# Optimization experiments

Hardware: AMD Instinct MI355X
Metric: run time of the kernel (lower is better)

## Reference

```python
import jax, jax.numpy as jnp
import numpy as np

B, T, H, V = 256, 256, 512, 32000
L = 3  # stacked LSTM layers


def setup_inputs() -> dict:
    key = jax.random.key(0)
    ks = jax.random.split(key, 12)
    s = 0.05
    n = lambda k, shp: (jax.random.normal(k, shp, jnp.float32) * s)
    return {
        "text_1": jax.random.randint(ks[0], (B, T), 0, V, dtype=jnp.int32),
        "text_2": jax.random.randint(ks[1], (B, T), 0, V, dtype=jnp.int32),
        "text_3": jax.random.randint(ks[2], (B, T), 0, V, dtype=jnp.int32),
        "emb": n(ks[3], (V, H)),
        "Wx": n(ks[4], (L, H, 4 * H)),
        "Wh": n(ks[5], (L, H, 4 * H)),
        "b": jnp.zeros((L, 4 * H), jnp.float32),
        "g1": jnp.ones((3 * H,), jnp.float32), "beta1": jnp.zeros((3 * H,), jnp.float32),
        "W1": n(ks[6], (3 * H, 2 * H)), "bd1": jnp.zeros((2 * H,), jnp.float32),
        "g2": jnp.ones((2 * H,), jnp.float32), "beta2": jnp.zeros((2 * H,), jnp.float32),
        "W2": n(ks[7], (2 * H, H // 5)), "bd2": jnp.zeros((H // 5,), jnp.float32),
        "g3": jnp.ones((H // 5,), jnp.float32), "beta3": jnp.zeros((H // 5,), jnp.float32),
        "W3": n(ks[8], (H // 5, 4)), "bd3": jnp.zeros((4,), jnp.float32),
    }


def _lstm_stack(tokens, emb, Wx, Wh, b):
    # tokens: [B, T] int -> last hidden of top layer [B, H]
    x = emb[tokens]                      # [B, T, H]
    x = jnp.transpose(x, (1, 0, 2))      # [T, B, H] (scan over time)
    bsz, h = x.shape[1], Wh.shape[1]
    for l in range(Wx.shape[0]):
        Wx_l, Wh_l, b_l = Wx[l], Wh[l], b[l]
        def step(carry, xt):
            hprev, cprev = carry
            gates = xt @ Wx_l + hprev @ Wh_l + b_l      # [B, 4H]
            i, f, g, o = jnp.split(gates, 4, axis=-1)
            c = jax.nn.sigmoid(f) * cprev + jax.nn.sigmoid(i) * jnp.tanh(g)
            hnew = jax.nn.sigmoid(o) * jnp.tanh(c)
            return (hnew, c), hnew
        init = (jnp.zeros((bsz, h), x.dtype), jnp.zeros((bsz, h), x.dtype))
        _, x = jax.lax.scan(step, init, x)
    return x[-1]                          # rnn_output[:, -1, :]


def _bn(x, gamma, beta, eps=1e-3):
    m = jnp.mean(x, axis=0)
    v = jnp.var(x, axis=0)
    return gamma * (x - m) * jax.lax.rsqrt(v + eps) + beta


def reference(text_1, text_2, text_3, emb, Wx, Wh, b,
              g1, beta1, W1, bd1, g2, beta2, W2, bd2, g3, beta3, W3, bd3):
    r1 = _lstm_stack(text_1, emb, Wx, Wh, b)
    r2 = _lstm_stack(text_2, emb, Wx, Wh, b)
    r3 = _lstm_stack(text_3, emb, Wx, Wh, b)
    r = jnp.concatenate([r1, r2, r3], axis=1)   # [B, 3H]
    r = _bn(r, g1, beta1)
    r = jax.nn.selu(r @ W1 + bd1)
    r = _bn(r, g2, beta2)
    r = jax.nn.selu(r @ W2 + bd2)
    r = _bn(r, g3, beta3)
    return r @ W3 + bd3                          # [B, 4] logits
```

## Files before the change

### kernel.cpp

```cpp
#include <hip/hip_runtime.h>
#include <hip/hip_bf16.h>

typedef __attribute__((ext_vector_type(8))) short short8;
typedef __attribute__((ext_vector_type(4))) float floatx4;

namespace {
constexpr int kB1 = 256;
constexpr int kT  = 256;
constexpr int kH  = 512;
constexpr int kL  = 3;
constexpr int kB3 = 768;
constexpr int kK  = 1024;
constexpr int kN  = 2048;
constexpr size_t kHB = (size_t)kB3 * kH;

constexpr size_t WREP_OFF   = 0;
constexpr size_t WREP_BYTES = (size_t)kL * kK * kN * 2;
constexpr size_t BREP_OFF   = WREP_OFF + WREP_BYTES;
constexpr size_t BREP_BYTES = (size_t)kL * kN * 4;
constexpr size_t HBUF_OFF   = BREP_OFF + BREP_BYTES;
constexpr size_t HBUF_BYTES = (size_t)kL * 2 * kHB * 2;
constexpr size_t CBUF_OFF   = HBUF_OFF + HBUF_BYTES;
constexpr size_t CBUF_BYTES = (size_t)kL * kHB * 4;
constexpr size_t BNA_OFF    = CBUF_OFF + CBUF_BYTES;
constexpr size_t BNC_OFF    = BNA_OFF + 1536 * 4;
constexpr size_t Z1_OFF     = BNC_OFF + 1536 * 4;
constexpr size_t Z2_OFF     = Z1_OFF + (size_t)256 * 1024 * 4;
constexpr size_t FLAG_OFF   = Z2_OFF + (size_t)256 * 102 * 4;
}

__device__ __forceinline__ float ldf(const void* p, size_t idx, int isf32) {
  if (isf32) return ((const float*)p)[idx];
  return __bfloat162float(((const __hip_bfloat16*)p)[idx]);
}

__device__ __forceinline__ short f2bs(float x) {
  union { __hip_bfloat16 h; short s; } u;
  u.h = __float2bfloat16(x);
  return u.s;
}

__global__ void detect_kernel(const unsigned* __restrict__ g1, int* __restrict__ flag) {
  if (threadIdx.x == 0 && blockIdx.x == 0)
    *flag = (g1[0] == 0x3F800000u) ? 1 : 0;
}

__global__ __launch_bounds__(256) void repack_kernel(
    const void* __restrict__ Wx, const void* __restrict__ Wh,
    const void* __restrict__ bias, const int* __restrict__ flagp,
    __hip_bfloat16* __restrict__ Wrep, float* __restrict__ brep) {
  int isf32 = *flagp;
  int idx = blockIdx.x * 256 + threadIdx.x;
  if (idx >= kL * kK * kN) return;
  int j  = idx & 7;
  int n2 = (idx >> 3) & (kN - 1);
  int kg = (idx >> 14) & 127;
  int l  = idx >> 21;
  int k  = kg * 8 + j;
  int ntile = n2 >> 7, c = n2 & 127, g = c >> 5, ul = c & 31;
  int u = ntile * 32 + ul;
  int col = g * 512 + u;
  float v;
  if (k < kH) v = ldf(Wx, ((size_t)l * kH + k) * kN + col, isf32);
  else        v = ldf(Wh, ((size_t)l * kH + (k - kH)) * kN + col, isf32);
  Wrep[idx] = __float2bfloat16(v);
  if (kg == 0 && j == 0) brep[l * kN + n2] = ldf(bias, (size_t)l * kN + col, isf32);
}

__global__ __launch_bounds__(256) void step_kernel(
    int s,
    const __hip_bfloat16* __restrict__ Wrep, const float* __restrict__ brep,
    __hip_bfloat16* __restrict__ hbuf, float* __restrict__ cbuf,
    const void* __restrict__ emb, const int* __restrict__ flagp,
    const int* __restrict__ t1, const int* __restrict__ t2, const int* __restrict__ t3) {
  __shared__ __align__(16) char smem[34816];

  int bid = blockIdx.x;
  int l  = bid / 192;
  int rr = bid % 192;
  int nt = rr & 15;
  int mt = rr >> 4;
  int t = s - l;
  if (t < 0 || t >= kT) return;

  int isf32 = *flagp;
  int tid = threadIdx.x;
  int wv = tid >> 6, lane = tid & 63;
  int lm = lane & 15, lq = lane >> 4;

  int arow = tid >> 2;
  int kc   = tid & 3;
  int row_g = mt * 64 + arow;

  const void* xsrc;
  bool xf32 = false;
  if (l == 0) {
    int i = row_g >> 8, bb = row_g & 255;
    const int* txt = (i == 0) ? t1 : (i == 1) ? t2 : t3;
    int tok = txt[bb * kT + t];
    if (isf32) { xsrc = (const void*)((const float*)emb + (size_t)tok * kH); xf32 = true; }
    else         xsrc = (const void*)((const __hip_bfloat16*)emb + (size_t)tok * kH);
  } else {
    const __hip_bfloat16* hIn = hbuf + ((size_t)(l - 1) * 2 + (t & 1)) * kHB;
    xsrc = (const void*)(hIn + (size_t)row_g * kH);
  }
  const __hip_bfloat16* hrow = nullptr;
  if (t > 0) {
    const __hip_bfloat16* hPrev = hbuf + ((size_t)l * 2 + ((t & 1) ^ 1)) * kHB;
    hrow = hPrev + (size_t)row_g * kH;
  }

  floatx4 zf = {0.f, 0.f, 0.f, 0.f};
  floatx4 acc[4][2];
#pragma unroll
  for (int a = 0; a < 4; a++)
#pragma unroll
    for (int b = 0; b < 2; b++) acc[a][b] = zf;

  const __hip_bfloat16* WB = Wrep + (size_t)l * kK * kN;
  int n0w = nt * 128 + wv * 32;

#pragma unroll 1
  for (int sl = 0; sl < 8; sl++) {
    short8 bfrag[4][2];
#pragma unroll
    for (int kk = 0; kk < 4; kk++)
#pragma unroll
      for (int nf = 0; nf < 2; nf++) {
        size_t kg = (size_t)(sl * 16 + kk * 4 + lq);
        const __hip_bfloat16* p = WB + (kg * kN + (n0w + nf * 16 + lm)) * 8;
        bfrag[kk][nf] = *(const short8*)p;
      }
    short8 av[4];
    bool zero = (sl >= 4) && (t == 0);
    if (!zero) {
      if (sl < 4 && xf32) {
        const float* sf = (const float*)xsrc + sl * 128;
#pragma unroll
        for (int jj = 0; jj < 4; jj++) {
          const float* q = sf + kc * 8 + jj * 32;
          float4 lo = *(const float4*)q;
          float4 hi = *(const float4*)(q + 4);
          short8 v;
          v[0] = f2bs(lo.x); v[1] = f2bs(lo.y); v[2] = f2bs(lo.z); v[3] = f2bs(lo.w);
          v[4] = f2bs(hi.x); v[5] = f2bs(hi.y); v[6] = f2bs(hi.z); v[7] = f2bs(hi.w);
          av[jj] = v;
        }
      } else {
        const __hip_bfloat16* src = (sl < 4)
            ? ((const __hip_bfloat16*)xsrc + sl * 128)
            : (hrow + (sl - 4) * 128);
#pragma unroll
        for (int jj = 0; jj < 4; jj++)
          av[jj] = *(const short8*)(src + kc * 8 + jj * 32);
      }
    } else {
      short8 vz = {0, 0, 0, 0, 0, 0, 0, 0};
#pragma unroll
      for (int jj = 0; jj < 4; jj++) av[jj] = vz;
    }
    __syncthreads();
#pragma unroll
    for (int jj = 0; jj < 4; jj++) {
      int klocal = kc * 8 + jj * 32;
      *(short8*)(smem + arow * 272 + klocal * 2) = av[jj];
    }
    __syncthreads();
#pragma unroll
    for (int kk = 0; kk < 4; kk++) {
      short8 afrag[4];
#pragma unroll
      for (int mf = 0; mf < 4; mf++) {
        int rowf = mf * 16 + lm;
        afrag[mf] = *(const short8*)(smem + rowf * 272 + kk * 64 + lq * 16);
      }
#pragma unroll
      for (int mf = 0; mf < 4; mf++)
#pragma unroll
        for (int nf = 0; nf < 2; nf++)
          acc[mf][nf] = __builtin_amdgcn_mfma_f32_16x16x32_bf16(
              afrag[mf], bfrag[kk][nf], acc[mf][nf], 0, 0, 0);
    }
  }

  const float* bl = brep + l * kN;
#pragma unroll
  for (int nf = 0; nf < 2; nf++) {
    float bv = bl[n0w + nf * 16 + lm];
#pragma unroll
    for (int mf = 0; mf < 4; mf++)
#pragma unroll
      for (int r = 0; r < 4; r++) acc[mf][nf][r] += bv;
  }

  __syncthreads();
  float* gl = (float*)smem;
#pragma unroll
  for (int mf = 0; mf < 4; mf++)
#pragma unroll
    for (int nf = 0; nf < 2; nf++)
#pragma unroll
      for (int r = 0; r < 4; r++) {
        int rowf = mf * 16 + lq * 4 + r;
        int uu   = nf * 16 + lm;
        gl[((size_t)wv * 64 + rowf) * 34 + uu] = acc[mf][nf][r];
      }
  __syncthreads();

  float* cl = cbuf + (size_t)l * kHB;
  __hip_bfloat16* hout = hbuf + ((size_t)l * 2 + (t & 1)) * kHB;
#pragma unroll
  for (int ii = 0; ii < 8; ii++) {
    int idx = tid + 256 * ii;
    int uu = idx & 31, rowf = idx >> 5;
    float gi = fminf(fmaxf(gl[(0 * 64 + rowf) * 34 + uu], -40.f), 40.f);
    float gf = fminf(fmaxf(gl[(1 * 64 + rowf) * 34 + uu], -40.f), 40.f);
    float gg = fminf(fmaxf(gl[(2 * 64 + rowf) * 34 + uu], -40.f), 40.f);
    float go = fminf(fmaxf(gl[(3 * 64 + rowf) * 34 + uu], -40.f), 40.f);
    int bg = mt * 64 + rowf;
    int ug = nt * 32 + uu;
    size_t off = (size_t)bg * kH + ug;
    float c_old = (t > 0) ? cl[off] : 0.f;
    float si = 1.f / (1.f + __expf(-gi));
    float sf = 1.f / (1.f + __expf(-gf));
    float so = 1.f / (1.f + __expf(-go));
    float cn = sf * c_old + si * tanhf(gg);
    float hn = so * tanhf(cn);
    cl[off] = cn;
    hout[off] = __float2bfloat16(hn);
  }
}

__global__ __launch_bounds__(256) void stats_kernel(
    int ncols, int mode, const void* __restrict__ src,
    const void* __restrict__ gamma, const void* __restrict__ beta,
    const int* __restrict__ flagp, float* __restrict__ bn_a, float* __restrict__ bn_c) {
  int isf32 = *flagp;
  int col = blockIdx.x * 256 + threadIdx.x;
  if (col >= ncols) return;
  float sum = 0.f, ss = 0.f;
  for (int b = 0; b < kB1; b++) {
    float v;
    if (mode == 0) {
      const __hip_bfloat16* h = (const __hip_bfloat16*)src;
      v = __bfloat162float(h[((size_t)((col >> 9) * kB1 + b)) * kH + (col & 511)]);
    } else {
      v = ((const float*)src)[(size_t)b * ncols + col];
    }
    v = fmaxf(-1e15f, fminf(v, 1e15f));
    sum += v; ss += v * v;
  }
  float mean = sum * (1.f / kB1);
  float var  = ss * (1.f / kB1) - mean * mean;
  float a = ldf(gamma, col, isf32) * rsqrtf(var + 1e-3f);
  bn_a[col] = a;
  bn_c[col] = ldf(beta, col, isf32) - mean * a;
}

__global__ __launch_bounds__(256) void headgemm_kernel(
    int Kd, int Nd, int mode, const void* __restrict__ Asrc,
    const float* __restrict__ bn_a, const float* __restrict__ bn_c,
    const void* __restrict__ W, const void* __restrict__ bias,
    const int* __restrict__ flagp, float* __restrict__ out, int do_selu) {
  __shared__ float As[32][65];
  __shared__ float Bs[32][65];
  int isf32 = *flagp;
  int tid = threadIdx.x;
  int bx = blockIdx.x, by = blockIdx.y;
  int tx = tid & 15, ty = tid >> 4;
  float acc[4][4] = {};
  int am = tid & 63, ak = tid >> 6;
  int bk = tid >> 3, bn8 = (tid & 7) * 8;
  for (int ks = 0; ks < Kd; ks += 32) {
    __syncthreads();
    for (int jj = 0; jj < 8; jj++) {
      int kl = ak * 8 + jj;
      int kg = ks + kl;
      int mg = by * 64 + am;
      float v;
      if (mode == 0) {
        const __hip_bfloat16* h = (const __hip_bfloat16*)Asrc;
        v = __bfloat162float(h[((size_t)((kg >> 9) * kB1 + mg)) * kH + (kg & 511)]);
      } else {
        v = ((const float*)Asrc)[(size_t)mg * Kd + kg];
      }
      As[kl][am] = v * bn_a[kg] + bn_c[kg];
    }
    for (int e = 0; e < 8; e++) {
      int col = bx * 64 + bn8 + e;
      Bs[bk][bn8 + e] = (col < Nd) ? ldf(W, (size_t)(ks + bk) * Nd + col, isf32) : 0.f;
    }
    __syncthreads();
    for (int k = 0; k < 32; k++) {
      float ar[4], br[4];
#pragma unroll
      for (int i = 0; i < 4; i++) ar[i] = As[k][ty * 4 + i];
#pragma unroll
      for (int j = 0; j < 4; j++) br[j] = Bs[k][tx * 4 + j];
#pragma unroll
      for (int i = 0; i < 4; i++)
#pragma unroll
        for (int j = 0; j < 4; j++) acc[i][j] += ar[i] * br[j];
    }
  }
  for (int i = 0; i < 4; i++) {
    int row = by * 64 + ty * 4 + i;
    for (int j = 0; j < 4; j++) {
      int col = bx * 64 + tx * 4 + j;
      if (col < Nd) {
        float y = acc[i][j] + ldf(bias, col, isf32);
        if (do_selu)
          y = (y > 0.f) ? 1.0507009873554805f * y
                        : 1.0507009873554805f * 1.6732632423543772f * (__expf(y) - 1.f);
        out[(size_t)row * Nd + col] = y;
      }
    }
  }
}

__global__ __launch_bounds__(256) void final_kernel(
    const float* __restrict__ z2, const float* __restrict__ bn_a, const float* __restrict__ bn_c,
    const void* __restrict__ W3, const void* __restrict__ bd3,
    const int* __restrict__ flagp, void* __restrict__ out) {
  int isf32 = *flagp;
  int b = threadIdx.x;
  float acc[4] = {0.f, 0.f, 0.f, 0.f};
  for (int j = 0; j < 102; j++) {
    float y = z2[b * 102 + j] * bn_a[j] + bn_c[j];
#pragma unroll
    for (int g = 0; g < 4; g++) acc[g] += y * ldf(W3, j * 4 + g, isf32);
  }
#pragma unroll
  for (int g = 0; g < 4; g++) {
    float y = acc[g] + ldf(bd3, g, isf32);
    if (isf32) ((float*)out)[b * 4 + g] = y;
    else ((__hip_bfloat16*)out)[b * 4 + g] = __float2bfloat16(y);
  }
}

extern "C" void kernel_launch(void* const* d_in, const int* in_sizes, int n_in,
                              void* d_out, int out_size, void* d_ws, size_t ws_size,
                              hipStream_t stream) {
  const int* t1 = (const int*)d_in[0];
  const int* t2 = (const int*)d_in[1];
  const int* t3 = (const int*)d_in[2];
  const void* emb = d_in[3];
  const void* Wx  = d_in[4];
  const void* Wh  = d_in[5];
  const void* bb  = d_in[6];
  const void* g1  = d_in[7];
  const void* be1 = d_in[8];
  const void* W1  = d_in[9];
  const void* bd1 = d_in[10];
  const void* g2  = d_in[11];
  const void* be2 = d_in[12];
  const void* W2  = d_in[13];
  const void* bd2 = d_in[14];
  const void* g3  = d_in[15];
  const void* be3 = d_in[16];
  const void* W3  = d_in[17];
  const void* bd3 = d_in[18];

  char* ws = (char*)d_ws;
  __hip_bfloat16* Wrep = (__hip_bfloat16*)(ws + WREP_OFF);
  float* brep = (float*)(ws + BREP_OFF);
  __hip_bfloat16* hbuf = (__hip_bfloat16*)(ws + HBUF_OFF);
  float* cbuf = (float*)(ws + CBUF_OFF);
  float* bn_a = (float*)(ws + BNA_OFF);
  float* bn_c = (float*)(ws + BNC_OFF);
  float* z1 = (float*)(ws + Z1_OFF);
  float* z2 = (float*)(ws + Z2_OFF);
  int* flag = (int*)(ws + FLAG_OFF);

  detect_kernel<<<1, 64, 0, stream>>>((const unsigned*)g1, flag);

  repack_kernel<<<(kL * kK * kN) / 256, 256, 0, stream>>>(Wx, Wh, bb, flag, Wrep, brep);

  for (int s = 0; s < kT + kL - 1; s++)
    step_kernel<<<3 * 192, 256, 0, stream>>>(s, Wrep, brep, hbuf, cbuf, emb, flag, t1, t2, t3);

  const __hip_bfloat16* hTop = hbuf + (2 * 2 + 1) * kHB;
  stats_kernel<<<6, 256, 0, stream>>>(1536, 0, hTop, g1, be1, flag, bn_a, bn_c);
  headgemm_kernel<<<dim3(16, 4), 256, 0, stream>>>(1536, 1024, 0, hTop, bn_a, bn_c, W1, bd1, flag, z1, 1);
  stats_kernel<<<4, 256, 0, stream>>>(1024, 1, z1, g2, be2, flag, bn_a, bn_c);
  headgemm_kernel<<<dim3(2, 4), 256, 0, stream>>>(1024, 102, 1, z1, bn_a, bn_c, W2, bd2, flag, z2, 1);
  stats_kernel<<<1, 256, 0, stream>>>(102, 1, z2, g3, be3, flag, bn_a, bn_c);
  final_kernel<<<1, 256, 0, stream>>>(z2, bn_a, bn_c, W3, bd3, flag, (void*)d_out);
}
```

Baseline: 6.078 ms.

## Replace per-timestep kernel launches with persistent kernel and grid barrier

Replaces the 258 per-wavefront step kernel launches with a single persistent kernel of 768 blocks that loops over time steps and synchronises through a hierarchical atomic grid barrier. The cell state is kept in registers instead of global memory, and hidden-state loads use coherent loads that bypass the caches. The goal is to remove launch overhead and cbuf traffic. In exchange it relies on all 768 blocks being co-resident, checked once through an occupancy query. The barrier has a timeout escape that could silently break correctness if it ever fires.

```diff
diff --git a/kernel.cpp b/kernel.cpp
--- a/kernel.cpp
+++ b/kernel.cpp
@@ -27,6 +27,8 @@
 constexpr size_t Z1_OFF     = BNC_OFF + 1536 * 4;
 constexpr size_t Z2_OFF     = Z1_OFF + (size_t)256 * 1024 * 4;
 constexpr size_t FLAG_OFF   = Z2_OFF + (size_t)256 * 102 * 4;
+constexpr size_t BAR_OFF    = FLAG_OFF + 128;
+constexpr int kPersistGrid  = 768;
 }
 
 __device__ __forceinline__ float ldf(const void* p, size_t idx, int isf32) {
@@ -40,8 +42,28 @@
   return u.s;
 }
 
-__global__ void detect_kernel(const unsigned* __restrict__ g1, int* __restrict__ flag) {
-  if (threadIdx.x == 0 && blockIdx.x == 0)
+__device__ __forceinline__ short8 cvt8(const float* q) {
+  float4 lo = *(const float4*)q;
+  float4 hi = *(const float4*)(q + 4);
+  short8 v;
+  v[0] = f2bs(lo.x); v[1] = f2bs(lo.y); v[2] = f2bs(lo.z); v[3] = f2bs(lo.w);
+  v[4] = f2bs(hi.x); v[5] = f2bs(hi.y); v[6] = f2bs(hi.z); v[7] = f2bs(hi.w);
+  return v;
+}
+
+__device__ __forceinline__ short8 ldg16_coh(const void* p) {
+  short8 v;
+  asm volatile("global_load_dwordx4 %0, %1, off sc0 sc1"
+               : "=v"(v) : "v"(p) : "memory");
+  return v;
+}
+
+__global__ void detect_kernel(const unsigned* __restrict__ g1, int* __restrict__ flag,
+                              unsigned* __restrict__ bar) {
+  int tid = threadIdx.x;
+  if (tid < 256)
+    __hip_atomic_store(&bar[tid], 0u, __ATOMIC_RELAXED, __HIP_MEMORY_SCOPE_AGENT);
+  if (tid == 0 && blockIdx.x == 0)
     *flag = (g1[0] == 0x3F800000u) ? 1 : 0;
 }
 
@@ -65,6 +87,204 @@
   else        v = ldf(Wh, ((size_t)l * kH + (k - kH)) * kN + col, isf32);
   Wrep[idx] = __float2bfloat16(v);
   if (kg == 0 && j == 0) brep[l * kN + n2] = ldf(bias, (size_t)l * kN + col, isf32);
+}
+
+__device__ __forceinline__ void grid_barrier(unsigned* bar, int bid, int tid) {
+  __syncthreads();
+  if (tid == 0) {
+    unsigned* cnt  = bar + (bid & 7) * 16;
+    unsigned* gcnt = bar + 128;
+    unsigned* gen  = bar + 160;
+    __threadfence();
+    unsigned g = __hip_atomic_load(gen, __ATOMIC_RELAXED, __HIP_MEMORY_SCOPE_AGENT);
+    unsigned a = __hip_atomic_fetch_add(cnt, 1u, __ATOMIC_ACQ_REL, __HIP_MEMORY_SCOPE_AGENT);
+    if (a == (kPersistGrid / 8) - 1u) {
+      __hip_atomic_store(cnt, 0u, __ATOMIC_RELAXED, __HIP_MEMORY_SCOPE_AGENT);
+      unsigned ga = __hip_atomic_fetch_add(gcnt, 1u, __ATOMIC_ACQ_REL, __HIP_MEMORY_SCOPE_AGENT);
+      if (ga == 7u) {
+        __hip_atomic_store(gcnt, 0u, __ATOMIC_RELAXED, __HIP_MEMORY_SCOPE_AGENT);
+        __hip_atomic_store(gen, g + 1u, __ATOMIC_RELEASE, __HIP_MEMORY_SCOPE_AGENT);
+      }
+    }
+    long long t0 = (long long)__builtin_amdgcn_s_memrealtime();
+    while (__hip_atomic_load(gen, __ATOMIC_ACQUIRE, __HIP_MEMORY_SCOPE_AGENT) == g) {
+      __builtin_amdgcn_s_sleep(2);
+      if ((long long)__builtin_amdgcn_s_memrealtime() - t0 > 20000000LL) break;
+    }
+  }
+  __syncthreads();
+}
+
+__global__ __launch_bounds__(256, 3) void persist_kernel(
+    const __hip_bfloat16* __restrict__ Wrep, const float* __restrict__ brep,
+    __hip_bfloat16* __restrict__ hbuf, const void* __restrict__ emb,
+    const int* __restrict__ flagp, const int* __restrict__ t1,
+    const int* __restrict__ t2, const int* __restrict__ t3,
+    unsigned* __restrict__ bar) {
+  __shared__ __align__(16) char smem[26624];
+
+  const int tid = threadIdx.x;
+  const int bid = blockIdx.x;
+  const int l   = bid >> 8;
+  const int mt  = (bid >> 4) & 15;
+  const int nt  = bid & 15;
+  const int wv = tid >> 6, lane = tid & 63, lm = lane & 15, lq = lane >> 4;
+  const int isf32 = *flagp;
+  const int r0   = tid >> 4;
+  const int kcol = (tid & 15) * 8;
+
+  const int R0 = mt * 48 + r0, R1 = R0 + 16, R2 = R0 + 32;
+  const int* tb0 = nullptr; const int* tb1 = nullptr; const int* tb2 = nullptr;
+  if (l == 0) {
+    tb0 = (((R0 >> 8) == 0) ? t1 : ((R0 >> 8) == 1) ? t2 : t3) + (R0 & 255) * kT;
+    tb1 = (((R1 >> 8) == 0) ? t1 : ((R1 >> 8) == 1) ? t2 : t3) + (R1 & 255) * kT;
+    tb2 = (((R2 >> 8) == 0) ? t1 : ((R2 >> 8) == 1) ? t2 : t3) + (R2 & 255) * kT;
+  }
+  const unsigned ro0 = (unsigned)R0 * kH + kcol;
+  const unsigned ro1 = (unsigned)R1 * kH + kcol;
+  const unsigned ro2 = (unsigned)R2 * kH + kcol;
+
+  const __hip_bfloat16* WB = Wrep + (size_t)l * kK * kN;
+  const int n0w = nt * 128 + wv * 32;
+  const float bv0 = brep[l * kN + n0w + lm];
+  const float bv1 = brep[l * kN + n0w + 16 + lm];
+
+  char* aw0 = smem + r0 * 272 + (tid & 15) * 16;
+  char* aw1 = aw0 + 16 * 272;
+  char* aw2 = aw0 + 32 * 272;
+  const char* ar = smem + lm * 272 + lq * 16;
+
+  const int cuu = tid & 31, crow = tid >> 5;
+  float creg[6] = {0.f, 0.f, 0.f, 0.f, 0.f, 0.f};
+
+#pragma unroll 1
+  for (int s = 0; s < kT + kL - 1; s++) {
+    const int t = s - l;
+    if (t >= 0 && t < kT) {
+      const __hip_bfloat16* hp = hbuf + ((size_t)l * 2 + ((t & 1) ^ 1)) * kHB;
+      const __hip_bfloat16* xh = nullptr;
+      const void *xe0 = nullptr, *xe1 = nullptr, *xe2 = nullptr;
+      if (l == 0) {
+        int k0 = tb0[t], k1 = tb1[t], k2 = tb2[t];
+        if (isf32) {
+          xe0 = (const void*)((const float*)emb + (size_t)k0 * kH + kcol);
+          xe1 = (const void*)((const float*)emb + (size_t)k1 * kH + kcol);
+          xe2 = (const void*)((const float*)emb + (size_t)k2 * kH + kcol);
+        } else {
+          xe0 = (const void*)((const __hip_bfloat16*)emb + (size_t)k0 * kH + kcol);
+          xe1 = (const void*)((const __hip_bfloat16*)emb + (size_t)k1 * kH + kcol);
+          xe2 = (const void*)((const __hip_bfloat16*)emb + (size_t)k2 * kH + kcol);
+        }
+      } else {
+        xh = hbuf + ((size_t)(l - 1) * 2 + (t & 1)) * kHB;
+      }
+
+      auto loadA = [&](int sl, short8& d0, short8& d1, short8& d2) {
+        if (sl < 4) {
+          if (l == 0) {
+            if (isf32) {
+              d0 = cvt8((const float*)xe0 + sl * 128);
+              d1 = cvt8((const float*)xe1 + sl * 128);
+              d2 = cvt8((const float*)xe2 + sl * 128);
+            } else {
+              d0 = *(const short8*)((const __hip_bfloat16*)xe0 + sl * 128);
+              d1 = *(const short8*)((const __hip_bfloat16*)xe1 + sl * 128);
+              d2 = *(const short8*)((const __hip_bfloat16*)xe2 + sl * 128);
+            }
+          } else {
+            d0 = ldg16_coh(xh + ro0 + sl * 128);
+            d1 = ldg16_coh(xh + ro1 + sl * 128);
+            d2 = ldg16_coh(xh + ro2 + sl * 128);
+          }
+        } else if (t == 0) {
+          short8 z = {0, 0, 0, 0, 0, 0, 0, 0};
+          d0 = z; d1 = z; d2 = z;
+        } else {
+          d0 = ldg16_coh(hp + ro0 + (sl - 4) * 128);
+          d1 = ldg16_coh(hp + ro1 + (sl - 4) * 128);
+          d2 = ldg16_coh(hp + ro2 + (sl - 4) * 128);
+        }
+      };
+
+      floatx4 zf = {0.f, 0.f, 0.f, 0.f};
+      floatx4 acc[3][2];
+#pragma unroll
+      for (int a = 0; a < 3; a++) { acc[a][0] = zf; acc[a][1] = zf; }
+
+      short8 avA0, avA1, avA2, avB0, avB1, avB2;
+      loadA(0, avA0, avA1, avA2);
+
+#pragma unroll
+      for (int sl = 0; sl < 8; sl++) {
+        __syncthreads();
+        asm volatile("s_waitcnt vmcnt(0)" ::: "memory");
+        if ((sl & 1) == 0) {
+          *(short8*)aw0 = avA0; *(short8*)aw1 = avA1; *(short8*)aw2 = avA2;
+          if (sl < 7) loadA(sl + 1, avB0, avB1, avB2);
+        } else {
+          *(short8*)aw0 = avB0; *(short8*)aw1 = avB1; *(short8*)aw2 = avB2;
+          if (sl < 7) loadA(sl + 1, avA0, avA1, avA2);
+        }
+        short8 bfrag[4][2];
+#pragma unroll
+        for (int kk = 0; kk < 4; kk++)
+#pragma unroll
+          for (int nf = 0; nf < 2; nf++) {
+            int kg = sl * 16 + kk * 4 + lq;
+            bfrag[kk][nf] = *(const short8*)(WB + ((size_t)kg * kN + n0w + nf * 16 + lm) * 8);
+          }
+        __syncthreads();
+#pragma unroll
+        for (int kk = 0; kk < 4; kk++) {
+          short8 af0 = *(const short8*)(ar + 0 * 4352 + kk * 64);
+          short8 af1 = *(const short8*)(ar + 1 * 4352 + kk * 64);
+          short8 af2 = *(const short8*)(ar + 2 * 4352 + kk * 64);
+          acc[0][0] = __builtin_amdgcn_mfma_f32_16x16x32_bf16(af0, bfrag[kk][0], acc[0][0], 0, 0, 0);
+          acc[0][1] = __builtin_amdgcn_mfma_f32_16x16x32_bf16(af0, bfrag[kk][1], acc[0][1], 0, 0, 0);
+          acc[1][0] = __builtin_amdgcn_mfma_f32_16x16x32_bf16(af1, bfrag[kk][0], acc[1][0], 0, 0, 0);
+          acc[1][1] = __builtin_amdgcn_mfma_f32_16x16x32_bf16(af1, bfrag[kk][1], acc[1][1], 0, 0, 0);
+          acc[2][0] = __builtin_amdgcn_mfma_f32_16x16x32_bf16(af2, bfrag[kk][0], acc[2][0], 0, 0, 0);
+          acc[2][1] = __builtin_amdgcn_mfma_f32_16x16x32_bf16(af2, bfrag[kk][1], acc[2][1], 0, 0, 0);
+        }
+      }
+
+      __syncthreads();
+      float* gl = (float*)smem;
+#pragma unroll
+      for (int mf = 0; mf < 3; mf++)
+#pragma unroll
+        for (int nf = 0; nf < 2; nf++)
+#pragma unroll
+          for (int r = 0; r < 4; r++) {
+            int rowf = mf * 16 + lq * 4 + r;
+            gl[(wv * 48 + rowf) * 34 + nf * 16 + lm] = acc[mf][nf][r] + (nf ? bv1 : bv0);
+          }
+      __syncthreads();
+
+      __hip_bfloat16* hout = hbuf + ((size_t)l * 2 + (t & 1)) * kHB;
+#pragma unroll
+      for (int ii = 0; ii < 6; ii++) {
+        int rowf = crow + 8 * ii;
+        float gi = fminf(fmaxf(gl[(0 * 48 + rowf) * 34 + cuu], -40.f), 40.f);
+        float gf = fminf(fmaxf(gl[(1 * 48 + rowf) * 34 + cuu], -40.f), 40.f);
+        float gg = fminf(fmaxf(gl[(2 * 48 + rowf) * 34 + cuu], -40.f), 40.f);
+        float go = fminf(fmaxf(gl[(3 * 48 + rowf) * 34 + cuu], -40.f), 40.f);
+        float c_old = (t > 0) ? creg[ii] : 0.f;
+        float si = 1.f / (1.f + __expf(-gi));
+        float sf = 1.f / (1.f + __expf(-gf));
+        float so = 1.f / (1.f + __expf(-go));
+        float cn = sf * c_old + si * tanhf(gg);
+        float hn = so * tanhf(cn);
+        creg[ii] = cn;
+        union { __hip_bfloat16 h; unsigned short u; } cv;
+        cv.h = __float2bfloat16(hn);
+        __hip_atomic_store(
+            (unsigned short*)(hout + (size_t)(mt * 48 + rowf) * kH + nt * 32 + cuu),
+            cv.u, __ATOMIC_RELAXED, __HIP_MEMORY_SCOPE_AGENT);
+      }
+    }
+    if (s < kT + kL - 2) grid_barrier(bar, bid, tid);
+  }
 }
 
 __global__ __launch_bounds__(256) void step_kernel(
@@ -371,13 +591,28 @@
   float* z1 = (float*)(ws + Z1_OFF);
   float* z2 = (float*)(ws + Z2_OFF);
   int* flag = (int*)(ws + FLAG_OFF);
-
-  detect_kernel<<<1, 64, 0, stream>>>((const unsigned*)g1, flag);
+  unsigned* bar = (unsigned*)(ws + BAR_OFF);
+
+  static int persist_ok = -1;
+  if (persist_ok < 0) {
+    int nb = 0, ncu = 0, dev = 0;
+    (void)hipGetDevice(&dev);
+    (void)hipDeviceGetAttribute(&ncu, hipDeviceAttributeMultiprocessorCount, dev);
+    hipError_t e = hipOccupancyMaxActiveBlocksPerMultiprocessor(&nb, persist_kernel, 256, 0);
+    persist_ok = (e == hipSuccess && (long)nb * (long)ncu >= kPersistGrid) ? 1 : 0;
+  }
+
+  detect_kernel<<<1, 256, 0, stream>>>((const unsigned*)g1, flag, bar);
 
   repack_kernel<<<(kL * kK * kN) / 256, 256, 0, stream>>>(Wx, Wh, bb, flag, Wrep, brep);
 
-  for (int s = 0; s < kT + kL - 1; s++)
-    step_kernel<<<3 * 192, 256, 0, stream>>>(s, Wrep, brep, hbuf, cbuf, emb, flag, t1, t2, t3);
+  if (persist_ok) {
+    persist_kernel<<<kPersistGrid, 256, 0, stream>>>(
+        Wrep, brep, hbuf, emb, flag, t1, t2, t3, bar);
+  } else {
+    for (int s = 0; s < kT + kL - 1; s++)
+      step_kernel<<<3 * 192, 256, 0, stream>>>(s, Wrep, brep, hbuf, cbuf, emb, flag, t1, t2, t3);
+  }
 
   const __hip_bfloat16* hTop = hbuf + (2 * 2 + 1) * kHB;
   stats_kernel<<<6, 256, 0, stream>>>(1536, 0, hTop, g1, be1, flag, bn_a, bn_c);
```

After: 6.054 ms. About the same (-0.4%).
